# Kernel optimization log

Measured on AMD Instinct MI355X. Metric: run time of the kernel, lower is better.

The kernel has to match this reference:

```python
import jax, jax.numpy as jnp
import numpy as np

B, N, D = 4, 64, 64          # batch, n_nodes, state_dim
FN, FE, INTER, T = 32, 16, 128, 3


def setup_inputs() -> dict:
    key = jax.random.key(0)
    ks = jax.random.split(key, 12)
    conn = (jax.random.uniform(ks[0], (B, N * N, 1)) < 0.3).astype(jnp.float32)
    feat = jax.random.uniform(ks[1], (B, N * N, FE - 1))
    edges = jnp.concatenate([conn, feat], axis=-1)
    nodes = jax.random.normal(ks[2], (B, N, FN))
    adjacency = jnp.zeros((B, N * N, 1))  # unused (adjacency=False)
    s = lambda i, sh, fan: jax.random.normal(ks[i], sh) * (1.0 / np.sqrt(fan))
    return dict(
        edges=edges, nodes=nodes, adjacency=adjacency,
        W_en=s(3, (FN, D), FN), b_en=jnp.zeros(D),
        W_agg=s(4, (FE, D * D), FE), b_agg=jnp.zeros(D * D),
        W_ih=s(5, (3 * D, D), D), W_hh=s(6, (3 * D, D), D),
        b_ih=jnp.zeros(3 * D), b_hh=jnp.zeros(3 * D),
        W_r1=s(7, (2 * D + FE, INTER), 2 * D + FE), b_r1=jnp.zeros(INTER),
        W_r2=s(8, (INTER, INTER), INTER), b_r2=jnp.zeros(INTER),
        W_r3=s(9, (INTER, 1), INTER), b_r3=jnp.zeros(1),
    )


def _gru_cell(x, h, W_ih, W_hh, b_ih, b_hh):
    # PyTorch nn.GRU cell: gates ordered (r, z, n)
    gi = x @ W_ih.T + b_ih
    gh = h @ W_hh.T + b_hh
    ir, iz, inn = jnp.split(gi, 3, axis=-1)
    hr, hz, hn = jnp.split(gh, 3, axis=-1)
    r = jax.nn.sigmoid(ir + hr)
    z = jax.nn.sigmoid(iz + hz)
    n = jnp.tanh(inn + r * hn)
    return (1.0 - z) * n + z * h


def reference(edges, nodes, adjacency, W_en, b_en, W_agg, b_agg,
              W_ih, W_hh, b_ih, b_hh, W_r1, b_r1, W_r2, b_r2, W_r3, b_r3):
    # mask: torch.where(x==0, x, ones) on first edge feature -> {0,1}
    mask = jnp.where(edges[..., :1] == 0, 0.0, 1.0)  # [B, N*N, 1]
    h = jax.nn.relu(nodes @ W_en + b_en)  # [B, N, D]
    for _ in range(T):
        # per-edge dynamic weight matrices A: [B, N*N, D, D]
        A = jax.nn.relu(edges @ W_agg + b_agg).reshape(B, N * N, D, D)
        node_j = jnp.tile(h, (1, N, 1))  # [B, N*N, D]
        msgs = jnp.einsum('beij,bej->bei', A, node_j) * mask  # [B, N*N, D]
        agg = msgs.reshape(B, N, N, D).sum(2)  # [B, N, D]
        hf = h.reshape(-1, D)
        af = agg.reshape(-1, D)
        # GRU over length-2 sequence [old_state, agg_messages], h0 = 0; take last
        h1 = _gru_cell(hf, jnp.zeros_like(hf), W_ih, W_hh, b_ih, b_hh)
        h2 = _gru_cell(af, h1, W_ih, W_hh, b_ih, b_hh)
        h = h2.reshape(B, N, D)
    # Readout over all node pairs
    state_i = jnp.repeat(h, N, axis=1)      # [B, N*N, D] (node i repeated)
    state_j = jnp.tile(h, (1, N, 1))        # [B, N*N, D]
    cat = jnp.concatenate([state_i, edges, state_j], axis=-1)
    a1 = jax.nn.relu(cat @ W_r1 + b_r1)
    a2 = jax.nn.relu(a1 @ W_r2 + b_r2)
    return a2 @ W_r3 + b_r3  # [B, N*N, 1]
```

## Files before the change

### kernel.cpp

```cpp
#include <hip/hip_runtime.h>

typedef float float4v __attribute__((ext_vector_type(4)));

__device__ __forceinline__ float sigm(float x) { return 1.0f / (1.0f + __expf(-x)); }

#define HS_LD 68

__global__ __launch_bounds__(1024) void k_it(
    const float* __restrict__ edges, const float* __restrict__ nodes,
    const float* __restrict__ W_en, const float* __restrict__ b_en,
    const float* __restrict__ W_agg, const float* __restrict__ b_agg,
    const float* __restrict__ W_ih, const float* __restrict__ W_hh,
    const float* __restrict__ b_ih, const float* __restrict__ b_hh,
    const float* __restrict__ h_cur, float* __restrict__ h_next,
    const float* __restrict__ W_r1, const float* __restrict__ b_r1,
    float* __restrict__ Ha, float* __restrict__ Hc, int it0, int emit)
{
    __shared__ float hs[64 * HS_LD];
    __shared__ float eL[64 * 16];
    __shared__ int   jn[64];
    __shared__ int   nES;
    __shared__ float xtra[768];

    int t = threadIdx.x;
    int row = blockIdx.x;
    int ri = row & 63;
    int b = row >> 6;

    if (it0) {
#pragma unroll
        for (int q = 0; q < 4; ++q) {
            int idx = q * 1024 + t;
            int n = idx >> 6, d = idx & 63;
            const float* np_ = nodes + ((b << 6) + n) * 32;
            float acc = b_en[d];
#pragma unroll
            for (int k = 0; k < 32; ++k)
                acc = fmaf(np_[k], W_en[k * 64 + d], acc);
            hs[n * HS_LD + d] = fmaxf(acc, 0.f);
        }
    } else {
        int n = t >> 4, col = (t & 15) * 4;
        *(float4v*)(hs + n * HS_LD + col) =
            *(const float4v*)(h_cur + ((b << 6) + n) * 64 + col);
    }

    if (t < 64) {
        const float* ep = edges + ((size_t)row * 64 + t) * 16;
        float f0 = ep[0];
        unsigned long long m = __ballot(f0 != 0.f);
        if (t == 0) nES = __popcll(m);
        if (f0 != 0.f) {
            int pos = __popcll(m & ((1ull << t) - 1ull));
            jn[pos] = t;
            float* dst = eL + pos * 16;
#pragma unroll
            for (int u = 0; u < 4; ++u)
                *(float4v*)(dst + u * 4) = *(const float4v*)(ep + u * 4);
        }
    }

    int dim = t >> 4, c4 = t & 15;
    float4v w[16];
    {
        const float* wp = W_agg + dim * 64 + c4 * 4;
#pragma unroll
        for (int k = 0; k < 16; ++k)
            w[k] = *(const float4v*)(wp + k * 4096);
    }
    float4v bias = *(const float4v*)(b_agg + dim * 64 + c4 * 4);

    __syncthreads();
    int nE = nES;

    float rsum = 0.f;
    for (int s = 0; s < nE; ++s) {
        const float* eP = eL + s * 16;
        float4v e0 = *(const float4v*)(eP);
        float4v e1 = *(const float4v*)(eP + 4);
        float4v e2 = *(const float4v*)(eP + 8);
        float4v e3 = *(const float4v*)(eP + 12);
        int ej = jn[s];
        float4v a = bias;
#pragma unroll
        for (int k = 0; k < 4; ++k) {
#pragma unroll
            for (int u = 0; u < 4; ++u) a[u] = fmaf(e0[k], w[k][u], a[u]);
        }
#pragma unroll
        for (int k = 0; k < 4; ++k) {
#pragma unroll
            for (int u = 0; u < 4; ++u) a[u] = fmaf(e1[k], w[4 + k][u], a[u]);
        }
#pragma unroll
        for (int k = 0; k < 4; ++k) {
#pragma unroll
            for (int u = 0; u < 4; ++u) a[u] = fmaf(e2[k], w[8 + k][u], a[u]);
        }
#pragma unroll
        for (int k = 0; k < 4; ++k) {
#pragma unroll
            for (int u = 0; u < 4; ++u) a[u] = fmaf(e3[k], w[12 + k][u], a[u]);
        }
        float4v hv = *(const float4v*)(hs + ej * HS_LD + c4 * 4);
#pragma unroll
        for (int u = 0; u < 4; ++u)
            rsum = fmaf(fmaxf(a[u], 0.f), hv[u], rsum);
    }
#pragma unroll
    for (int m = 1; m < 16; m <<= 1) rsum += __shfl_xor(rsum, m, 64);
    float* aggS = xtra;
    if (c4 == 0) aggS[dim] = rsum;
    __syncthreads();

    float* g1  = xtra + 64;
    float* h1S = xtra + 256;
    float* g2i = xtra + 320;
    float* g2h = xtra + 512;
    float* hnS = xtra + 704;
    const float* hrow = hs + ri * HS_LD;

    if (t < 192) {
        float g = b_ih[t];
        const float* wr = W_ih + t * 64;
#pragma unroll
        for (int k = 0; k < 64; ++k) g = fmaf(hrow[k], wr[k], g);
        g1[t] = g;
    }
    __syncthreads();
    if (t < 64) {
        float r1 = sigm(g1[t] + b_hh[t]);
        float z1 = sigm(g1[64 + t] + b_hh[64 + t]);
        float nn1 = tanhf(g1[128 + t] + r1 * b_hh[128 + t]);
        h1S[t] = (1.f - z1) * nn1;
    }
    __syncthreads();
    if (t < 192) {
        float gi = b_ih[t];
        float gh = b_hh[t];
        const float* wri = W_ih + t * 64;
        const float* wrh = W_hh + t * 64;
#pragma unroll
        for (int k = 0; k < 64; ++k) {
            gi = fmaf(aggS[k], wri[k], gi);
            gh = fmaf(h1S[k], wrh[k], gh);
        }
        g2i[t] = gi; g2h[t] = gh;
    }
    __syncthreads();
    if (t < 64) {
        float r = sigm(g2i[t] + g2h[t]);
        float z = sigm(g2i[64 + t] + g2h[64 + t]);
        float nn = tanhf(g2i[128 + t] + r * g2h[128 + t]);
        float hn = (1.f - z) * nn + z * h1S[t];
        h_next[row * 64 + t] = hn;
        hnS[t] = hn;
    }
    __syncthreads();
    if (emit && t < 256) {
        int m = t >> 7, d = t & 127;
        const float* wbase = W_r1 + (m ? 80 * 128 : 0) + d;
        float acc = m ? 0.f : b_r1[d];
#pragma unroll
        for (int k = 0; k < 64; ++k)
            acc = fmaf(hnS[k], wbase[k * 128], acc);
        if (m == 0) Ha[row * 128 + d] = acc;
        else        Hc[row * 128 + d] = acc;
    }
}

__global__ __launch_bounds__(256) void k_read(
    const float* __restrict__ edges,
    const float* __restrict__ Ha, const float* __restrict__ Hc,
    const float* __restrict__ W_r1,
    const float* __restrict__ W_r2, const float* __restrict__ b_r2,
    const float* __restrict__ W_r3, const float* __restrict__ b_r3,
    float* __restrict__ out)
{
    __shared__ float HaS[128];
    __shared__ float eS[32 * 16];
    __shared__ float A1[32 * 128];
    int t = threadIdx.x;
    int unit = blockIdx.x;
    int row = unit >> 1, qp = unit & 1;
    int b = row >> 6;

    const float* src = Hc + (size_t)((b << 6) + qp * 32) * 128;
#pragma unroll
    for (int r = 0; r < 4; ++r) {
        int off = (r * 256 + t) * 4;
        *(float4v*)(A1 + off) = *(const float4v*)(src + off);
    }
    if (t < 32)
        *(float4v*)(HaS + t * 4) = *(const float4v*)(Ha + (size_t)row * 128 + t * 4);
    if (t < 128)
        *(float4v*)(eS + t * 4) =
            *(const float4v*)(edges + ((size_t)row * 64 + qp * 32) * 16 + t * 4);
    __syncthreads();

    int td = t & 31, pg = t >> 5;

    float4v ew0 = {0,0,0,0}, ew1 = ew0, ew2 = ew0, ew3 = ew0;
#pragma unroll
    for (int k = 0; k < 16; ++k) {
        float4v wk = *(const float4v*)(W_r1 + (64 + k) * 128 + td * 4);
        float e0 = eS[(pg * 4 + 0) * 16 + k];
        float e1 = eS[(pg * 4 + 1) * 16 + k];
        float e2 = eS[(pg * 4 + 2) * 16 + k];
        float e3 = eS[(pg * 4 + 3) * 16 + k];
#pragma unroll
        for (int u = 0; u < 4; ++u) {
            ew0[u] = fmaf(e0, wk[u], ew0[u]);
            ew1[u] = fmaf(e1, wk[u], ew1[u]);
            ew2[u] = fmaf(e2, wk[u], ew2[u]);
            ew3[u] = fmaf(e3, wk[u], ew3[u]);
        }
    }
    float4v ha = *(const float4v*)(HaS + td * 4);
#pragma unroll
    for (int pi = 0; pi < 4; ++pi) {
        float4v ew = (pi == 0) ? ew0 : (pi == 1) ? ew1 : (pi == 2) ? ew2 : ew3;
        float* slot = A1 + (pg * 4 + pi) * 128 + td * 4;
        float4v hc = *(const float4v*)slot;
        float4v a;
#pragma unroll
        for (int u = 0; u < 4; ++u) a[u] = fmaxf(hc[u] + ha[u] + ew[u], 0.f);
        *(float4v*)slot = a;
    }
    __syncthreads();

    float4v bb2 = *(const float4v*)(b_r2 + td * 4);
    float4v acc0 = bb2, acc1 = bb2, acc2 = bb2, acc3 = bb2;
    for (int k4 = 0; k4 < 32; ++k4) {
        float4v wA = *(const float4v*)(W_r2 + (k4 * 4 + 0) * 128 + td * 4);
        float4v wB = *(const float4v*)(W_r2 + (k4 * 4 + 1) * 128 + td * 4);
        float4v wC = *(const float4v*)(W_r2 + (k4 * 4 + 2) * 128 + td * 4);
        float4v wD = *(const float4v*)(W_r2 + (k4 * 4 + 3) * 128 + td * 4);
        float4v a0 = *(const float4v*)(A1 + (pg * 4 + 0) * 128 + k4 * 4);
        float4v a1 = *(const float4v*)(A1 + (pg * 4 + 1) * 128 + k4 * 4);
        float4v a2 = *(const float4v*)(A1 + (pg * 4 + 2) * 128 + k4 * 4);
        float4v a3 = *(const float4v*)(A1 + (pg * 4 + 3) * 128 + k4 * 4);
#pragma unroll
        for (int u = 0; u < 4; ++u) {
            acc0[u] = fmaf(a0[0], wA[u], acc0[u]);
            acc0[u] = fmaf(a0[1], wB[u], acc0[u]);
            acc0[u] = fmaf(a0[2], wC[u], acc0[u]);
            acc0[u] = fmaf(a0[3], wD[u], acc0[u]);
            acc1[u] = fmaf(a1[0], wA[u], acc1[u]);
            acc1[u] = fmaf(a1[1], wB[u], acc1[u]);
            acc1[u] = fmaf(a1[2], wC[u], acc1[u]);
            acc1[u] = fmaf(a1[3], wD[u], acc1[u]);
            acc2[u] = fmaf(a2[0], wA[u], acc2[u]);
            acc2[u] = fmaf(a2[1], wB[u], acc2[u]);
            acc2[u] = fmaf(a2[2], wC[u], acc2[u]);
            acc2[u] = fmaf(a2[3], wD[u], acc2[u]);
            acc3[u] = fmaf(a3[0], wA[u], acc3[u]);
            acc3[u] = fmaf(a3[1], wB[u], acc3[u]);
            acc3[u] = fmaf(a3[2], wC[u], acc3[u]);
            acc3[u] = fmaf(a3[3], wD[u], acc3[u]);
        }
    }

    float4v w3v = *(const float4v*)(W_r3 + td * 4);
    float b3 = b_r3[0];
    float p0 = fmaxf(acc0[0], 0.f) * w3v[0] + fmaxf(acc0[1], 0.f) * w3v[1]
             + fmaxf(acc0[2], 0.f) * w3v[2] + fmaxf(acc0[3], 0.f) * w3v[3];
    float p1 = fmaxf(acc1[0], 0.f) * w3v[0] + fmaxf(acc1[1], 0.f) * w3v[1]
             + fmaxf(acc1[2], 0.f) * w3v[2] + fmaxf(acc1[3], 0.f) * w3v[3];
    float p2 = fmaxf(acc2[0], 0.f) * w3v[0] + fmaxf(acc2[1], 0.f) * w3v[1]
             + fmaxf(acc2[2], 0.f) * w3v[2] + fmaxf(acc2[3], 0.f) * w3v[3];
    float p3 = fmaxf(acc3[0], 0.f) * w3v[0] + fmaxf(acc3[1], 0.f) * w3v[1]
             + fmaxf(acc3[2], 0.f) * w3v[2] + fmaxf(acc3[3], 0.f) * w3v[3];
#pragma unroll
    for (int m = 1; m < 32; m <<= 1) {
        p0 += __shfl_xor(p0, m, 64);
        p1 += __shfl_xor(p1, m, 64);
        p2 += __shfl_xor(p2, m, 64);
        p3 += __shfl_xor(p3, m, 64);
    }
    if (td == 0) {
        int obase = row * 64 + qp * 32 + pg * 4;
        out[obase + 0] = p0 + b3;
        out[obase + 1] = p1 + b3;
        out[obase + 2] = p2 + b3;
        out[obase + 3] = p3 + b3;
    }
}

extern "C" void kernel_launch(void* const* d_in, const int* in_sizes, int n_in,
                              void* d_out, int out_size, void* d_ws, size_t ws_size,
                              hipStream_t stream)
{
    const float* edges = (const float*)d_in[0];
    const float* nodes = (const float*)d_in[1];
    const float* W_en  = (const float*)d_in[3];
    const float* b_en  = (const float*)d_in[4];
    const float* W_agg = (const float*)d_in[5];
    const float* b_agg = (const float*)d_in[6];
    const float* W_ih  = (const float*)d_in[7];
    const float* W_hh  = (const float*)d_in[8];
    const float* b_ih  = (const float*)d_in[9];
    const float* b_hh  = (const float*)d_in[10];
    const float* W_r1  = (const float*)d_in[11];
    const float* b_r1  = (const float*)d_in[12];
    const float* W_r2  = (const float*)d_in[13];
    const float* b_r2  = (const float*)d_in[14];
    const float* W_r3  = (const float*)d_in[15];
    const float* b_r3  = (const float*)d_in[16];

    float* hA = (float*)d_ws;
    float* hB = hA + 16384;
    float* Ha = hB + 16384;
    float* Hc = Ha + 256 * 128;
    float* out = (float*)d_out;

    k_it<<<256, 1024, 0, stream>>>(edges, nodes, W_en, b_en, W_agg, b_agg,
                                   W_ih, W_hh, b_ih, b_hh, hA, hA,
                                   W_r1, b_r1, Ha, Hc, 1, 0);
    k_it<<<256, 1024, 0, stream>>>(edges, nodes, W_en, b_en, W_agg, b_agg,
                                   W_ih, W_hh, b_ih, b_hh, hA, hB,
                                   W_r1, b_r1, Ha, Hc, 0, 0);
    k_it<<<256, 1024, 0, stream>>>(edges, nodes, W_en, b_en, W_agg, b_agg,
                                   W_ih, W_hh, b_ih, b_hh, hB, hA,
                                   W_r1, b_r1, Ha, Hc, 0, 1);
    k_read<<<512, 256, 0, stream>>>(edges, Ha, Hc, W_r1, W_r2, b_r2,
                                    W_r3, b_r3, out);
}
```

Before: 83.19 us.

## Overlap GRU input gates with edge loop, unroll it, and split readout finer

In the iteration kernel, the first GRU input-gate matvec (which depends only on the old node state) now runs before the edge-message loop instead of after it, which removes one barrier and lets the two overlap across waves. The edge loop is also unrolled by two. The readout kernel now handles 16 pairs per block instead of 32, doubling the grid to 1024 blocks with fewer accumulators per thread. The aim is more parallelism and less serialization, at the cost of reloading the W_r2 weights twice as often across blocks.

```diff
diff --git a/kernel.cpp b/kernel.cpp
--- a/kernel.cpp
+++ b/kernel.cpp
@@ -73,46 +73,7 @@
     __syncthreads();
     int nE = nES;
 
-    float rsum = 0.f;
-    for (int s = 0; s < nE; ++s) {
-        const float* eP = eL + s * 16;
-        float4v e0 = *(const float4v*)(eP);
-        float4v e1 = *(const float4v*)(eP + 4);
-        float4v e2 = *(const float4v*)(eP + 8);
-        float4v e3 = *(const float4v*)(eP + 12);
-        int ej = jn[s];
-        float4v a = bias;
-#pragma unroll
-        for (int k = 0; k < 4; ++k) {
-#pragma unroll
-            for (int u = 0; u < 4; ++u) a[u] = fmaf(e0[k], w[k][u], a[u]);
-        }
-#pragma unroll
-        for (int k = 0; k < 4; ++k) {
-#pragma unroll
-            for (int u = 0; u < 4; ++u) a[u] = fmaf(e1[k], w[4 + k][u], a[u]);
-        }
-#pragma unroll
-        for (int k = 0; k < 4; ++k) {
-#pragma unroll
-            for (int u = 0; u < 4; ++u) a[u] = fmaf(e2[k], w[8 + k][u], a[u]);
-        }
-#pragma unroll
-        for (int k = 0; k < 4; ++k) {
-#pragma unroll
-            for (int u = 0; u < 4; ++u) a[u] = fmaf(e3[k], w[12 + k][u], a[u]);
-        }
-        float4v hv = *(const float4v*)(hs + ej * HS_LD + c4 * 4);
-#pragma unroll
-        for (int u = 0; u < 4; ++u)
-            rsum = fmaf(fmaxf(a[u], 0.f), hv[u], rsum);
-    }
-#pragma unroll
-    for (int m = 1; m < 16; m <<= 1) rsum += __shfl_xor(rsum, m, 64);
     float* aggS = xtra;
-    if (c4 == 0) aggS[dim] = rsum;
-    __syncthreads();
-
     float* g1  = xtra + 64;
     float* h1S = xtra + 256;
     float* g2i = xtra + 320;
@@ -127,7 +88,56 @@
         for (int k = 0; k < 64; ++k) g = fmaf(hrow[k], wr[k], g);
         g1[t] = g;
     }
-    __syncthreads();
+
+    float rsum = 0.f;
+#define EDGE_BODY(SLOT)                                                        \
+    {                                                                          \
+        const float* eP = eL + (SLOT) * 16;                                    \
+        float4v e0 = *(const float4v*)(eP);                                    \
+        float4v e1 = *(const float4v*)(eP + 4);                                \
+        float4v e2 = *(const float4v*)(eP + 8);                                \
+        float4v e3 = *(const float4v*)(eP + 12);                               \
+        int ej = jn[(SLOT)];                                                   \
+        float4v a = bias;                                                      \
+        _Pragma("unroll")                                                      \
+        for (int k = 0; k < 4; ++k) {                                          \
+            _Pragma("unroll")                                                  \
+            for (int u = 0; u < 4; ++u) a[u] = fmaf(e0[k], w[k][u], a[u]);     \
+        }                                                                      \
+        _Pragma("unroll")                                                      \
+        for (int k = 0; k < 4; ++k) {                                          \
+            _Pragma("unroll")                                                  \
+            for (int u = 0; u < 4; ++u) a[u] = fmaf(e1[k], w[4 + k][u], a[u]); \
+        }                                                                      \
+        _Pragma("unroll")                                                      \
+        for (int k = 0; k < 4; ++k) {                                          \
+            _Pragma("unroll")                                                  \
+            for (int u = 0; u < 4; ++u) a[u] = fmaf(e2[k], w[8 + k][u], a[u]); \
+        }                                                                      \
+        _Pragma("unroll")                                                      \
+        for (int k = 0; k < 4; ++k) {                                          \
+            _Pragma("unroll")                                                  \
+            for (int u = 0; u < 4; ++u) a[u] = fmaf(e3[k], w[12 + k][u], a[u]);\
+        }                                                                      \
+        float4v hv = *(const float4v*)(hs + ej * HS_LD + c4 * 4);              \
+        _Pragma("unroll")                                                      \
+        for (int u = 0; u < 4; ++u)                                            \
+            rsum = fmaf(fmaxf(a[u], 0.f), hv[u], rsum);                        \
+    }
+
+    int s = 0;
+    for (; s + 2 <= nE; s += 2) {
+        EDGE_BODY(s);
+        EDGE_BODY(s + 1);
+    }
+    if (s < nE) EDGE_BODY(s);
+#undef EDGE_BODY
+
+#pragma unroll
+    for (int m = 1; m < 16; m <<= 1) rsum += __shfl_xor(rsum, m, 64);
+    if (c4 == 0) aggS[dim] = rsum;
+    __syncthreads();
+
     if (t < 64) {
         float r1 = sigm(g1[t] + b_hh[t]);
         float z1 = sigm(g1[64 + t] + b_hh[64 + t]);
@@ -178,49 +188,45 @@
     float* __restrict__ out)
 {
     __shared__ float HaS[128];
-    __shared__ float eS[32 * 16];
-    __shared__ float A1[32 * 128];
+    __shared__ float eS[16 * 16];
+    __shared__ float A1[16 * 128];
     int t = threadIdx.x;
     int unit = blockIdx.x;
-    int row = unit >> 1, qp = unit & 1;
+    int row = unit >> 2, qp = unit & 3;
     int b = row >> 6;
 
-    const float* src = Hc + (size_t)((b << 6) + qp * 32) * 128;
-#pragma unroll
-    for (int r = 0; r < 4; ++r) {
+    const float* src = Hc + (size_t)((b << 6) + qp * 16) * 128;
+#pragma unroll
+    for (int r = 0; r < 2; ++r) {
         int off = (r * 256 + t) * 4;
         *(float4v*)(A1 + off) = *(const float4v*)(src + off);
     }
     if (t < 32)
         *(float4v*)(HaS + t * 4) = *(const float4v*)(Ha + (size_t)row * 128 + t * 4);
-    if (t < 128)
+    if (t < 64)
         *(float4v*)(eS + t * 4) =
-            *(const float4v*)(edges + ((size_t)row * 64 + qp * 32) * 16 + t * 4);
+            *(const float4v*)(edges + ((size_t)row * 64 + qp * 16) * 16 + t * 4);
     __syncthreads();
 
     int td = t & 31, pg = t >> 5;
 
-    float4v ew0 = {0,0,0,0}, ew1 = ew0, ew2 = ew0, ew3 = ew0;
+    float4v ew0 = {0,0,0,0}, ew1 = ew0;
 #pragma unroll
     for (int k = 0; k < 16; ++k) {
         float4v wk = *(const float4v*)(W_r1 + (64 + k) * 128 + td * 4);
-        float e0 = eS[(pg * 4 + 0) * 16 + k];
-        float e1 = eS[(pg * 4 + 1) * 16 + k];
-        float e2 = eS[(pg * 4 + 2) * 16 + k];
-        float e3 = eS[(pg * 4 + 3) * 16 + k];
+        float e0 = eS[(pg * 2 + 0) * 16 + k];
+        float e1 = eS[(pg * 2 + 1) * 16 + k];
 #pragma unroll
         for (int u = 0; u < 4; ++u) {
             ew0[u] = fmaf(e0, wk[u], ew0[u]);
             ew1[u] = fmaf(e1, wk[u], ew1[u]);
-            ew2[u] = fmaf(e2, wk[u], ew2[u]);
-            ew3[u] = fmaf(e3, wk[u], ew3[u]);
         }
     }
     float4v ha = *(const float4v*)(HaS + td * 4);
 #pragma unroll
-    for (int pi = 0; pi < 4; ++pi) {
-        float4v ew = (pi == 0) ? ew0 : (pi == 1) ? ew1 : (pi == 2) ? ew2 : ew3;
-        float* slot = A1 + (pg * 4 + pi) * 128 + td * 4;
+    for (int pi = 0; pi < 2; ++pi) {
+        float4v ew = pi ? ew1 : ew0;
+        float* slot = A1 + (pg * 2 + pi) * 128 + td * 4;
         float4v hc = *(const float4v*)slot;
         float4v a;
 #pragma unroll
@@ -230,16 +236,14 @@
     __syncthreads();
 
     float4v bb2 = *(const float4v*)(b_r2 + td * 4);
-    float4v acc0 = bb2, acc1 = bb2, acc2 = bb2, acc3 = bb2;
+    float4v acc0 = bb2, acc1 = bb2;
     for (int k4 = 0; k4 < 32; ++k4) {
         float4v wA = *(const float4v*)(W_r2 + (k4 * 4 + 0) * 128 + td * 4);
         float4v wB = *(const float4v*)(W_r2 + (k4 * 4 + 1) * 128 + td * 4);
         float4v wC = *(const float4v*)(W_r2 + (k4 * 4 + 2) * 128 + td * 4);
         float4v wD = *(const float4v*)(W_r2 + (k4 * 4 + 3) * 128 + td * 4);
-        float4v a0 = *(const float4v*)(A1 + (pg * 4 + 0) * 128 + k4 * 4);
-        float4v a1 = *(const float4v*)(A1 + (pg * 4 + 1) * 128 + k4 * 4);
-        float4v a2 = *(const float4v*)(A1 + (pg * 4 + 2) * 128 + k4 * 4);
-        float4v a3 = *(const float4v*)(A1 + (pg * 4 + 3) * 128 + k4 * 4);
+        float4v a0 = *(const float4v*)(A1 + (pg * 2 + 0) * 128 + k4 * 4);
+        float4v a1 = *(const float4v*)(A1 + (pg * 2 + 1) * 128 + k4 * 4);
 #pragma unroll
         for (int u = 0; u < 4; ++u) {
             acc0[u] = fmaf(a0[0], wA[u], acc0[u]);
@@ -250,14 +254,6 @@
             acc1[u] = fmaf(a1[1], wB[u], acc1[u]);
             acc1[u] = fmaf(a1[2], wC[u], acc1[u]);
             acc1[u] = fmaf(a1[3], wD[u], acc1[u]);
-            acc2[u] = fmaf(a2[0], wA[u], acc2[u]);
-            acc2[u] = fmaf(a2[1], wB[u], acc2[u]);
-            acc2[u] = fmaf(a2[2], wC[u], acc2[u]);
-            acc2[u] = fmaf(a2[3], wD[u], acc2[u]);
-            acc3[u] = fmaf(a3[0], wA[u], acc3[u]);
-            acc3[u] = fmaf(a3[1], wB[u], acc3[u]);
-            acc3[u] = fmaf(a3[2], wC[u], acc3[u]);
-            acc3[u] = fmaf(a3[3], wD[u], acc3[u]);
         }
     }
 
@@ -267,23 +263,15 @@
              + fmaxf(acc0[2], 0.f) * w3v[2] + fmaxf(acc0[3], 0.f) * w3v[3];
     float p1 = fmaxf(acc1[0], 0.f) * w3v[0] + fmaxf(acc1[1], 0.f) * w3v[1]
              + fmaxf(acc1[2], 0.f) * w3v[2] + fmaxf(acc1[3], 0.f) * w3v[3];
-    float p2 = fmaxf(acc2[0], 0.f) * w3v[0] + fmaxf(acc2[1], 0.f) * w3v[1]
-             + fmaxf(acc2[2], 0.f) * w3v[2] + fmaxf(acc2[3], 0.f) * w3v[3];
-    float p3 = fmaxf(acc3[0], 0.f) * w3v[0] + fmaxf(acc3[1], 0.f) * w3v[1]
-             + fmaxf(acc3[2], 0.f) * w3v[2] + fmaxf(acc3[3], 0.f) * w3v[3];
 #pragma unroll
     for (int m = 1; m < 32; m <<= 1) {
         p0 += __shfl_xor(p0, m, 64);
         p1 += __shfl_xor(p1, m, 64);
-        p2 += __shfl_xor(p2, m, 64);
-        p3 += __shfl_xor(p3, m, 64);
     }
     if (td == 0) {
-        int obase = row * 64 + qp * 32 + pg * 4;
+        int obase = row * 64 + qp * 16 + pg * 2;
         out[obase + 0] = p0 + b3;
         out[obase + 1] = p1 + b3;
-        out[obase + 2] = p2 + b3;
-        out[obase + 3] = p3 + b3;
     }
 }
 
@@ -323,6 +311,6 @@
     k_it<<<256, 1024, 0, stream>>>(edges, nodes, W_en, b_en, W_agg, b_agg,
                                    W_ih, W_hh, b_ih, b_hh, hB, hA,
                                    W_r1, b_r1, Ha, Hc, 0, 1);
-    k_read<<<512, 256, 0, stream>>>(edges, Ha, Hc, W_r1, W_r2, b_r2,
-                                    W_r3, b_r3, out);
+    k_read<<<1024, 256, 0, stream>>>(edges, Ha, Hc, W_r1, W_r2, b_r2,
+                                     W_r3, b_r3, out);
 }
```

Measured after the change: 85.17 us. 2.4% more time.
